# Kernel tuning notes

Measured on AMD Instinct MI355X. Metric: run time of the kernel, lower is better.

Reference implementation:

```python
import jax, jax.numpy as jnp
import numpy as np

B, T, C = 4, 2048, 1024
NH = 16
HS = C // NH


def setup_inputs() -> dict:
    key = jax.random.key(0)
    k1, k2, k3, k4, k5 = jax.random.split(key, 5)
    scale = 1.0 / np.sqrt(C)
    return {
        "x": jax.random.normal(k1, (B, T, C), dtype=jnp.float32),
        "Wk": jax.random.normal(k2, (C, C), dtype=jnp.float32) * scale,
        "Wq": jax.random.normal(k3, (C, C), dtype=jnp.float32) * scale,
        "Wv": jax.random.normal(k4, (C, C), dtype=jnp.float32) * scale,
        "Wp": jax.random.normal(k5, (C, C), dtype=jnp.float32) * scale,
    }


def reference(x, Wk, Wq, Wv, Wp):
    b, t, c = x.shape
    # projections (nn.Linear with bias=False computes x @ W.T; weights here are
    # stored so that x @ W is equivalent -- same math, random init either way)
    k = (x @ Wk).reshape(b, t, NH, HS).transpose(0, 2, 1, 3)  # [B,H,T,hs]
    q = (x @ Wq).reshape(b, t, NH, HS).transpose(0, 2, 1, 3)
    v = (x @ Wv).reshape(b, t, NH, HS).transpose(0, 2, 1, 3)
    att = jnp.einsum("bhqd,bhkd->bhqk", q, k) / jnp.sqrt(jnp.float32(HS))
    causal = jnp.tril(jnp.ones((t, t), dtype=bool))
    att = jnp.where(causal[None, None, :, :], att, -jnp.inf)
    att = jax.nn.softmax(att, axis=-1)
    y = jnp.einsum("bhqk,bhkd->bhqd", att, v)  # [B,H,T,hs]
    y = y.transpose(0, 2, 1, 3).reshape(b, t, c)
    return y @ Wp
```

## Files before the change

kernel.cpp:

```cpp
#include <hip/hip_runtime.h>
#include <cstddef>
#include <cstdint>


namespace {

typedef unsigned short u16;
typedef unsigned int u32;
typedef __attribute__((ext_vector_type(8))) short s8v;
typedef __attribute__((ext_vector_type(4))) short s4v;
typedef __attribute__((ext_vector_type(4))) float f4v;

constexpr int Bn = 4, Tn = 2048, Cn = 1024;
constexpr int Mn = Bn * Tn;
constexpr int KVB = 128;
constexpr int NT128 = Tn / 128;
constexpr float QSCALE = 0.125f * 1.44269504f;

__device__ __forceinline__ u16 bfc(float f) {
  return __builtin_bit_cast(u16, (__bf16)f);
}

__device__ __forceinline__ float ex2(float x) {
#if __has_builtin(__builtin_amdgcn_exp2f)
  return __builtin_amdgcn_exp2f(x);
#else
  return exp2f(x);
#endif
}

__device__ __forceinline__ f4v mfma16(s8v a, s8v b, f4v c) {
  return __builtin_amdgcn_mfma_f32_16x16x32_bf16(a, b, c, 0, 0, 0);
}

__device__ __forceinline__ f4v mfma16k16(s4v a, s4v b, f4v c) {
#if __has_builtin(__builtin_amdgcn_mfma_f32_16x16x16bf16_1k)
  return __builtin_amdgcn_mfma_f32_16x16x16bf16_1k(a, b, c, 0, 0, 0);
#else
  f4v d = c;
  asm("v_mfma_f32_16x16x16_bf16 %0, %1, %2, %0" : "+v"(d) : "v"(a), "v"(b));
  return d;
#endif
}

typedef __attribute__((address_space(1))) const u32 gas_u32;
typedef __attribute__((address_space(3))) u32 las_u32;
__device__ __forceinline__ void gl_lds16(const void* g, void* l) {
  __builtin_amdgcn_global_load_lds((gas_u32*)g, (las_u32*)l, 16, 0, 0);
}

__global__ __launch_bounds__(256) void prep(
    const float* __restrict__ x, u16* __restrict__ xb,
    const float* __restrict__ w0, const float* __restrict__ w1,
    const float* __restrict__ w2, const float* __restrict__ w3,
    u16* __restrict__ o0, u16* __restrict__ o1, u16* __restrict__ o2,
    u16* __restrict__ o3) {
  __shared__ float Tsh[64][65];
  const int bid = blockIdx.x;
  const int tid = threadIdx.x;
  if (bid < 4096) {
    const size_t i = ((size_t)bid * 256 + tid) * 8;
    const float4 a = *(const float4*)(x + i);
    const float4 b = *(const float4*)(x + i + 4);
    alignas(16) u16 t[8] = {bfc(a.x), bfc(a.y), bfc(a.z), bfc(a.w),
                            bfc(b.x), bfc(b.y), bfc(b.z), bfc(b.w)};
    *(s8v*)(xb + i) = *(const s8v*)t;
    return;
  }
  const int idx = bid - 4096;
  const int wz = idx >> 8, wy = (idx >> 4) & 15, wx = idx & 15;
  const float* W;
  u16* O;
  switch (wz) {
    case 0: W = w0; O = o0; break;
    case 1: W = w1; O = o1; break;
    case 2: W = w2; O = o2; break;
    default: W = w3; O = o3; break;
  }
  const int n0 = wx * 64, k0 = wy * 64;
  {
    const int rk = tid >> 2, c0 = (tid & 3) * 16;
#pragma unroll
    for (int u = 0; u < 4; ++u) {
      const float4 v = *(const float4*)&W[(size_t)(k0 + rk) * Cn + n0 + c0 + u * 4];
      Tsh[rk][c0 + u * 4 + 0] = v.x;
      Tsh[rk][c0 + u * 4 + 1] = v.y;
      Tsh[rk][c0 + u * 4 + 2] = v.z;
      Tsh[rk][c0 + u * 4 + 3] = v.w;
    }
  }
  __syncthreads();
  {
    const int rn = tid >> 2, ck0 = (tid & 3) * 16;
    alignas(16) u16 t[16];
#pragma unroll
    for (int u = 0; u < 16; ++u) t[u] = bfc(Tsh[ck0 + u][rn]);
    *(s8v*)&O[(size_t)(n0 + rn) * Cn + k0 + ck0] = *(const s8v*)&t[0];
    *(s8v*)&O[(size_t)(n0 + rn) * Cn + k0 + ck0 + 8] = *(const s8v*)&t[8];
  }
}

template <int OUT_MODE>
__device__ __forceinline__ void gemm_body(const u16* __restrict__ A,
                                          const u16* __restrict__ Bt,
                                          void* __restrict__ Cout, int bm,
                                          int bn, u16* As, u16* Bs) {
  const int N = Cn, K = Cn;
  const int tid = threadIdx.x;
  const int l = tid & 63, w = tid >> 6;
  const int lr = l & 15, lh = l >> 4;
  const int wm = (w >> 1) * 64, wn = (w & 1) * 64;
  const u16* Ab = A + (size_t)(bm * 128) * K;
  const u16* Bb = Bt + (size_t)(bn * 128) * K;
  const int sw = lr & 7;
  f4v acc[4][4] = {};
  for (int k0 = 0; k0 < K; k0 += 64) {
    __syncthreads();
#pragma unroll
    for (int i = 0; i < 4; ++i) {
      const int s = tid + 256 * i;
      const int r = s >> 3, c = s & 7;
      gl_lds16(Ab + (size_t)r * K + k0 + ((c ^ (r & 7)) * 8), &As[s * 8]);
    }
#pragma unroll
    for (int i = 0; i < 4; ++i) {
      const int s = tid + 256 * i;
      const int r = s >> 3, c = s & 7;
      gl_lds16(Bb + (size_t)r * K + k0 + ((c ^ (r & 7)) * 8), &Bs[s * 8]);
    }
    __syncthreads();
#pragma unroll
    for (int half = 0; half < 2; ++half) {
      s8v af[4], bfr[4];
#pragma unroll
      for (int i = 0; i < 4; ++i)
        af[i] = *(const s8v*)&As[(wm + i * 16 + lr) * 64 +
                                 (((half * 4 + lh) ^ sw) * 8)];
#pragma unroll
      for (int j = 0; j < 4; ++j)
        bfr[j] = *(const s8v*)&Bs[(wn + j * 16 + lr) * 64 +
                                  (((half * 4 + lh) ^ sw) * 8)];
      __builtin_amdgcn_s_setprio(1);
#pragma unroll
      for (int i = 0; i < 4; ++i)
#pragma unroll
        for (int j = 0; j < 4; ++j)
          acc[i][j] = mfma16(af[i], bfr[j], acc[i][j]);
      __builtin_amdgcn_s_setprio(0);
    }
  }
  if (OUT_MODE == 2) {
    float* Cf = (float*)Cout;
#pragma unroll
    for (int i = 0; i < 4; ++i) {
      const int row = bm * 128 + wm + i * 16 + lh * 4;
#pragma unroll
      for (int j = 0; j < 4; ++j) {
        const int col = bn * 128 + wn + j * 16 + lr;
#pragma unroll
        for (int r = 0; r < 4; ++r)
          Cf[(size_t)(row + r) * N + col] = acc[i][j][r];
      }
    }
  } else if (OUT_MODE == 0 || OUT_MODE == 3) {
    u16* Cb = (u16*)Cout;
    const float sc = (OUT_MODE == 3) ? QSCALE : 1.0f;
#pragma unroll
    for (int i = 0; i < 4; ++i) {
      const int row = bm * 128 + wm + i * 16 + lh * 4;
#pragma unroll
      for (int j = 0; j < 4; ++j) {
        const int col = bn * 128 + wn + j * 16 + lr;
#pragma unroll
        for (int r = 0; r < 4; ++r)
          Cb[(size_t)(row + r) * N + col] = bfc(acc[i][j][r] * sc);
      }
    }
  } else {
    u16* Vt = (u16*)Cout;
#pragma unroll
    for (int i = 0; i < 4; ++i) {
      const int row0 = bm * 128 + wm + i * 16 + lh * 4;
      const int bq = row0 >> 11;
      const int t0g = row0 & 2047;
      const int tau = t0g & 127;
      const int taup = ((tau >> 5) << 5) | (((tau >> 2) & 3) << 3) |
                       (((tau >> 4) & 1) << 2);
      const int t0p = (t0g & ~127) | taup;
#pragma unroll
      for (int j = 0; j < 4; ++j) {
        const int col = bn * 128 + wn + j * 16 + lr;
        const int hh = col >> 6, dd = col & 63;
        alignas(8) u16 t4[4];
#pragma unroll
        for (int r = 0; r < 4; ++r) t4[r] = bfc(acc[i][j][r]);
        *(s4v*)&Vt[((size_t)((bq * 16 + hh) * 64 + dd)) * Tn + t0p] =
            *(const s4v*)t4;
      }
    }
  }
}

__global__ __launch_bounds__(256) void gemm_qkv(
    const u16* __restrict__ A, const u16* __restrict__ btq,
    const u16* __restrict__ btk, const u16* __restrict__ btv,
    u16* __restrict__ qb, u16* __restrict__ kb, u16* __restrict__ vt) {
  __shared__ __align__(16) u16 As[8192], Bs[8192];
  const int bid = blockIdx.x;
  const int xcd = bid & 7, j = bid >> 3;
  const int bm = xcd * 8 + (j & 7);
  const int combo = j >> 3;
  const int which = combo >> 3, bn = combo & 7;
  if (which == 0)
    gemm_body<3>(A, btq, qb, bm, bn, As, Bs);
  else if (which == 1)
    gemm_body<0>(A, btk, kb, bm, bn, As, Bs);
  else
    gemm_body<1>(A, btv, vt, bm, bn, As, Bs);
}

template <int OUT_MODE>
__global__ __launch_bounds__(256) void gemm_bt(const u16* __restrict__ A,
                                               const u16* __restrict__ Bt,
                                               void* __restrict__ Cout) {
  __shared__ __align__(16) u16 As[8192], Bs[8192];
  const int bid = blockIdx.x;
  const int xcd = bid & 7, j = bid >> 3;
  const int bm = xcd * 8 + (j & 7);
  const int bn = j >> 3;
  gemm_body<OUT_MODE>(A, Bt, Cout, bm, bn, As, Bs);
}

__device__ __forceinline__ void stage_kv(const u16* __restrict__ kgb,
                                         const u16* __restrict__ vtb,
                                         u16* __restrict__ Kb,
                                         u16* __restrict__ Vb, int k0,
                                         int tid) {
#pragma unroll
  for (int is = 0; is < 2; ++is) {
    const int slot = is * 512 + tid;
    const int row = slot >> 3, ch = slot & 7;
    gl_lds16(kgb + (size_t)(k0 + row) * Cn + ((ch ^ (row & 7)) * 8),
             &Kb[slot * 8]);
  }
#pragma unroll
  for (int is = 0; is < 2; ++is) {
    const int slot = is * 512 + tid;
    const int d = slot >> 4, ch = slot & 15;
    gl_lds16(vtb + (size_t)d * Tn + k0 + ((ch ^ (d & 7)) * 8), &Vb[slot * 8]);
  }
}

__device__ __forceinline__ void attn_step(const s8v (&aq)[2],
                                          const u16* __restrict__ Ks,
                                          const u16* __restrict__ Vs, int kb0,
                                          int kb1, const int (&vch)[4], int ln,
                                          int lh, bool diag, int k0, int qg,
                                          float& m_i, float& l_i, f4v* o) {
  f4v s[8] = {};
  __builtin_amdgcn_s_setprio(1);
#pragma unroll
  for (int n = 0; n < 8; ++n) {
    const s8v bk0 = *(const s8v*)&Ks[kb0 + n * 1024];
    const s8v bk1 = *(const s8v*)&Ks[kb1 + n * 1024];
    s[n] = mfma16(bk0, aq[0], s[n]);
    s[n] = mfma16(bk1, aq[1], s[n]);
  }
  __builtin_amdgcn_s_setprio(0);
  float rm = -1e30f;
  if (diag) {
#pragma unroll
    for (int n = 0; n < 8; ++n)
#pragma unroll
      for (int r = 0; r < 4; ++r) {
        float x = s[n][r];
        if (k0 + n * 16 + lh * 4 + r > qg) x = -1e30f;
        s[n][r] = x;
        rm = fmaxf(rm, x);
      }
  } else {
#pragma unroll
    for (int n = 0; n < 8; ++n)
      rm = fmaxf(rm, fmaxf(fmaxf(s[n][0], s[n][1]), fmaxf(s[n][2], s[n][3])));
  }
  if (!__all(rm <= m_i + 11.5f)) {
    float rr = fmaxf(rm, __shfl_xor(rm, 16));
    rr = fmaxf(rr, __shfl_xor(rr, 32));
    const float mnew = fmaxf(m_i, rr);
    const float al = ex2(m_i - mnew);
    m_i = mnew;
    l_i *= al;
#pragma unroll
    for (int r = 0; r < 4; ++r) {
      const float ar = __shfl(al, (ln & 48) | (lh * 4 + r));
#pragma unroll
      for (int n2 = 0; n2 < 4; ++n2) o[n2][r] *= ar;
    }
  }
  s4v pa[8];
  float rs = 0.f;
#pragma unroll
  for (int n = 0; n < 8; ++n) {
    const float p0 = ex2(s[n][0] - m_i);
    const float p1 = ex2(s[n][1] - m_i);
    const float p2 = ex2(s[n][2] - m_i);
    const float p3 = ex2(s[n][3] - m_i);
    rs += (p0 + p1) + (p2 + p3);
    pa[n] = (s4v){(short)bfc(p0), (short)bfc(p1), (short)bfc(p2),
                  (short)bfc(p3)};
  }
  l_i += rs;
  __builtin_amdgcn_s_setprio(1);
#pragma unroll
  for (int n2 = 0; n2 < 4; ++n2) {
#pragma unroll
    for (int p = 0; p < 4; ++p) {
      const s8v vv = *(const s8v*)&Vs[vch[p] + n2 * 2048];
      const s4v lo = {vv[0], vv[1], vv[2], vv[3]};
      const s4v hi = {vv[4], vv[5], vv[6], vv[7]};
      o[n2] = mfma16k16(pa[2 * p], lo, o[n2]);
      o[n2] = mfma16k16(pa[2 * p + 1], hi, o[n2]);
    }
  }
  __builtin_amdgcn_s_setprio(0);
}

__global__ __launch_bounds__(512) void attn_big(const u16* __restrict__ qg,
                                                const u16* __restrict__ kg,
                                                const u16* __restrict__ vtg,
                                                u16* __restrict__ yg) {
  __shared__ __align__(16) u16 Ks0[KVB * 64], Ks1[KVB * 64];
  __shared__ __align__(16) u16 Vs0[64 * KVB], Vs1[64 * KVB];
  const int tid = threadIdx.x;
  const int ln = tid & 63, w = tid >> 6;
  const int lr = ln & 15, lh = ln >> 4;
  const int bid = blockIdx.x;
  const int wg = (bid & 7) * 64 + (bid >> 3);
  const int bh = wg >> 3, xp = wg & 7;
  const int b = bh >> 4, h = bh & 15;
  const int tL = xp, tH = NT128 - 1 - xp;
  const int q0L = tL * 128, q0H = tH * 128;
  const u16* kgb = kg + (size_t)(b * Tn) * Cn + h * 64;
  const u16* vtb = vtg + (size_t)(bh * 64) * Tn;
  const int kb0 = lr * 64 + ((lh) ^ (lr & 7)) * 8;
  const int kb1 = lr * 64 + ((4 + lh) ^ (lr & 7)) * 8;
  int vch[4];
#pragma unroll
  for (int p = 0; p < 4; ++p)
    vch[p] = lr * 128 + ((p * 4 + lh) ^ (lr & 7)) * 8;
  s8v aqL[2], aqH[2];
  {
    const int row = w * 16 + lr;
#pragma unroll
    for (int kd = 0; kd < 2; ++kd) {
      aqL[kd] = *(const s8v*)&qg[(size_t)(b * Tn + q0L + row) * Cn + h * 64 +
                                 kd * 32 + lh * 8];
      aqH[kd] = *(const s8v*)&qg[(size_t)(b * Tn + q0H + row) * Cn + h * 64 +
                                 kd * 32 + lh * 8];
    }
  }
  const int qgH = q0H + w * 16 + lr;
  const int qgL = q0L + w * 16 + lr;
  float mL = -1e30f, lL = 0.f, mH = -1e30f, lH = 0.f;
  f4v oL[4] = {}, oH[4] = {};
  stage_kv(kgb, vtb, Ks0, Vs0, 0, tid);
  __syncthreads();
  for (int kt = 0; kt <= tH; ++kt) {
    const bool cur = kt & 1;
    const u16* Kb = cur ? Ks1 : Ks0;
    const u16* Vb = cur ? Vs1 : Vs0;
    if (kt < tH)
      stage_kv(kgb, vtb, cur ? Ks0 : Ks1, cur ? Vs0 : Vs1, (kt + 1) * KVB,
               tid);
    attn_step(aqH, Kb, Vb, kb0, kb1, vch, ln, lh, kt == tH, kt * KVB, qgH, mH,
              lH, oH);
    if (kt <= tL)
      attn_step(aqL, Kb, Vb, kb0, kb1, vch, ln, lh, kt == tL, kt * KVB, qgL,
                mL, lL, oL);
    __syncthreads();
  }
  {
    float ls = lH;
    ls += __shfl_xor(ls, 16);
    ls += __shfl_xor(ls, 32);
    const float linv = 1.0f / ls;
#pragma unroll
    for (int r = 0; r < 4; ++r) {
      const float iv = __shfl(linv, (ln & 48) | (lh * 4 + r));
      const int row = q0H + w * 16 + lh * 4 + r;
#pragma unroll
      for (int n2 = 0; n2 < 4; ++n2)
        yg[(size_t)(b * Tn + row) * Cn + h * 64 + n2 * 16 + lr] =
            bfc(oH[n2][r] * iv);
    }
  }
  {
    float ls = lL;
    ls += __shfl_xor(ls, 16);
    ls += __shfl_xor(ls, 32);
    const float linv = 1.0f / ls;
#pragma unroll
    for (int r = 0; r < 4; ++r) {
      const float iv = __shfl(linv, (ln & 48) | (lh * 4 + r));
      const int row = q0L + w * 16 + lh * 4 + r;
#pragma unroll
      for (int n2 = 0; n2 < 4; ++n2)
        yg[(size_t)(b * Tn + row) * Cn + h * 64 + n2 * 16 + lr] =
            bfc(oL[n2][r] * iv);
    }
  }
}

}

extern "C" void kernel_launch(void* const* d_in, const int* in_sizes, int n_in,
                              void* d_out, int out_size, void* d_ws,
                              size_t ws_size, hipStream_t stream) {
  (void)in_sizes; (void)n_in; (void)out_size; (void)ws_size;
  const float* x = (const float*)d_in[0];
  const float* Wk = (const float*)d_in[1];
  const float* Wq = (const float*)d_in[2];
  const float* Wv = (const float*)d_in[3];
  const float* Wp = (const float*)d_in[4];
  float* out = (float*)d_out;
  char* ws = (char*)d_ws;

  u16* xb = (u16*)(ws);
  u16* wqt = (u16*)(ws + 16777216);
  u16* wkt = (u16*)(ws + 18874368);
  u16* wvt = (u16*)(ws + 20971520);
  u16* wpt = (u16*)(ws + 23068672);
  u16* qb = (u16*)(ws + 25165824);
  u16* kb = (u16*)(ws + 41943040);
  u16* vt = (u16*)(ws + 58720256);
  u16* yb = (u16*)(ws + 75497472);

  prep<<<dim3(5120), dim3(256), 0, stream>>>(x, xb, Wq, Wk, Wv, Wp, wqt, wkt,
                                             wvt, wpt);
  gemm_qkv<<<dim3(1536), dim3(256), 0, stream>>>(xb, wqt, wkt, wvt, qb, kb,
                                                 vt);
  attn_big<<<dim3(512), dim3(512), 0, stream>>>(qb, kb, vt, yb);
  gemm_bt<2><<<dim3(512), dim3(256), 0, stream>>>(yb, wpt, out);
}
```

Measured before the change: 169.0 us.

## Split paired-tile attention into one query tile per block with 64-key KV tiles

The attention kernel previously had each block handle a low and a high query tile together, sharing 128-key KV tiles between them. Now each block handles one 128-row query tile and streams 64-key K/V tiles, so the grid doubles to 1024 blocks. Blocks are ordered so each XCD group gets a balanced mix of short and long causal tiles. This raises parallelism and halves LDS per block, at the cost of loading K/V once per query tile instead of sharing it across the pair. It also adds more loop iterations and barriers, and the diagonal masking now covers two 64-key tiles.

```diff
diff --git a/kernel.cpp b/kernel.cpp
--- a/kernel.cpp
+++ b/kernel.cpp
@@ -13,8 +13,6 @@
 
 constexpr int Bn = 4, Tn = 2048, Cn = 1024;
 constexpr int Mn = Bn * Tn;
-constexpr int KVB = 128;
-constexpr int NT128 = Tn / 128;
 constexpr float QSCALE = 0.125f * 1.44269504f;
 
 __device__ __forceinline__ u16 bfc(float f) {
@@ -236,31 +234,23 @@
                                          u16* __restrict__ Kb,
                                          u16* __restrict__ Vb, int k0,
                                          int tid) {
-#pragma unroll
-  for (int is = 0; is < 2; ++is) {
-    const int slot = is * 512 + tid;
-    const int row = slot >> 3, ch = slot & 7;
-    gl_lds16(kgb + (size_t)(k0 + row) * Cn + ((ch ^ (row & 7)) * 8),
-             &Kb[slot * 8]);
-  }
-#pragma unroll
-  for (int is = 0; is < 2; ++is) {
-    const int slot = is * 512 + tid;
-    const int d = slot >> 4, ch = slot & 15;
-    gl_lds16(vtb + (size_t)d * Tn + k0 + ((ch ^ (d & 7)) * 8), &Vb[slot * 8]);
-  }
+  const int row = tid >> 3, ch = tid & 7;
+  gl_lds16(kgb + (size_t)(k0 + row) * Cn + ((ch ^ (row & 7)) * 8),
+           &Kb[tid * 8]);
+  gl_lds16(vtb + (size_t)row * Tn + k0 + ((ch ^ (row & 7)) * 8),
+           &Vb[tid * 8]);
 }
 
 __device__ __forceinline__ void attn_step(const s8v (&aq)[2],
                                           const u16* __restrict__ Ks,
                                           const u16* __restrict__ Vs, int kb0,
-                                          int kb1, const int (&vch)[4], int ln,
+                                          int kb1, const int (&vch)[2], int ln,
                                           int lh, bool diag, int k0, int qg,
                                           float& m_i, float& l_i, f4v* o) {
-  f4v s[8] = {};
+  f4v s[4] = {};
   __builtin_amdgcn_s_setprio(1);
 #pragma unroll
-  for (int n = 0; n < 8; ++n) {
+  for (int n = 0; n < 4; ++n) {
     const s8v bk0 = *(const s8v*)&Ks[kb0 + n * 1024];
     const s8v bk1 = *(const s8v*)&Ks[kb1 + n * 1024];
     s[n] = mfma16(bk0, aq[0], s[n]);
@@ -270,7 +260,7 @@
   float rm = -1e30f;
   if (diag) {
 #pragma unroll
-    for (int n = 0; n < 8; ++n)
+    for (int n = 0; n < 4; ++n)
 #pragma unroll
       for (int r = 0; r < 4; ++r) {
         float x = s[n][r];
@@ -280,7 +270,7 @@
       }
   } else {
 #pragma unroll
-    for (int n = 0; n < 8; ++n)
+    for (int n = 0; n < 4; ++n)
       rm = fmaxf(rm, fmaxf(fmaxf(s[n][0], s[n][1]), fmaxf(s[n][2], s[n][3])));
   }
   if (!__all(rm <= m_i + 11.5f)) {
@@ -297,116 +287,98 @@
       for (int n2 = 0; n2 < 4; ++n2) o[n2][r] *= ar;
     }
   }
-  s4v pa[8];
   float rs = 0.f;
-#pragma unroll
-  for (int n = 0; n < 8; ++n) {
-    const float p0 = ex2(s[n][0] - m_i);
-    const float p1 = ex2(s[n][1] - m_i);
-    const float p2 = ex2(s[n][2] - m_i);
-    const float p3 = ex2(s[n][3] - m_i);
-    rs += (p0 + p1) + (p2 + p3);
-    pa[n] = (s4v){(short)bfc(p0), (short)bfc(p1), (short)bfc(p2),
-                  (short)bfc(p3)};
-  }
-  l_i += rs;
   __builtin_amdgcn_s_setprio(1);
 #pragma unroll
-  for (int n2 = 0; n2 < 4; ++n2) {
-#pragma unroll
-    for (int p = 0; p < 4; ++p) {
-      const s8v vv = *(const s8v*)&Vs[vch[p] + n2 * 2048];
+  for (int p = 0; p < 2; ++p) {
+    const float a0 = ex2(s[2 * p][0] - m_i);
+    const float a1 = ex2(s[2 * p][1] - m_i);
+    const float a2 = ex2(s[2 * p][2] - m_i);
+    const float a3 = ex2(s[2 * p][3] - m_i);
+    const float b0 = ex2(s[2 * p + 1][0] - m_i);
+    const float b1 = ex2(s[2 * p + 1][1] - m_i);
+    const float b2 = ex2(s[2 * p + 1][2] - m_i);
+    const float b3 = ex2(s[2 * p + 1][3] - m_i);
+    rs += ((a0 + a1) + (a2 + a3)) + ((b0 + b1) + (b2 + b3));
+    const s4v pa0 = {(short)bfc(a0), (short)bfc(a1), (short)bfc(a2),
+                     (short)bfc(a3)};
+    const s4v pa1 = {(short)bfc(b0), (short)bfc(b1), (short)bfc(b2),
+                     (short)bfc(b3)};
+#pragma unroll
+    for (int n2 = 0; n2 < 4; ++n2) {
+      const s8v vv = *(const s8v*)&Vs[vch[p] + n2 * 1024];
       const s4v lo = {vv[0], vv[1], vv[2], vv[3]};
       const s4v hi = {vv[4], vv[5], vv[6], vv[7]};
-      o[n2] = mfma16k16(pa[2 * p], lo, o[n2]);
-      o[n2] = mfma16k16(pa[2 * p + 1], hi, o[n2]);
+      o[n2] = mfma16k16(pa0, lo, o[n2]);
+      o[n2] = mfma16k16(pa1, hi, o[n2]);
     }
   }
   __builtin_amdgcn_s_setprio(0);
+  l_i += rs;
 }
 
 __global__ __launch_bounds__(512) void attn_big(const u16* __restrict__ qg,
                                                 const u16* __restrict__ kg,
                                                 const u16* __restrict__ vtg,
                                                 u16* __restrict__ yg) {
-  __shared__ __align__(16) u16 Ks0[KVB * 64], Ks1[KVB * 64];
-  __shared__ __align__(16) u16 Vs0[64 * KVB], Vs1[64 * KVB];
+  __shared__ __align__(16) u16 Ks0[4096], Ks1[4096];
+  __shared__ __align__(16) u16 Vs0[4096], Vs1[4096];
   const int tid = threadIdx.x;
   const int ln = tid & 63, w = tid >> 6;
   const int lr = ln & 15, lh = ln >> 4;
   const int bid = blockIdx.x;
-  const int wg = (bid & 7) * 64 + (bid >> 3);
-  const int bh = wg >> 3, xp = wg & 7;
+  const int wg = (bid & 7) * 128 + (bid >> 3);
+  const int xcd = wg >> 7, gl = (wg >> 5) & 3, r5 = wg & 31;
+  const int qt = (gl & 1) ? (15 - (r5 & 7)) : (r5 & 7);
+  const int bh = ((gl >> 1) << 5) | (xcd << 2) | (r5 >> 3);
   const int b = bh >> 4, h = bh & 15;
-  const int tL = xp, tH = NT128 - 1 - xp;
-  const int q0L = tL * 128, q0H = tH * 128;
+  const int q0 = qt * 128;
+  const int nlast = 2 * qt + 1;
   const u16* kgb = kg + (size_t)(b * Tn) * Cn + h * 64;
   const u16* vtb = vtg + (size_t)(bh * 64) * Tn;
   const int kb0 = lr * 64 + ((lh) ^ (lr & 7)) * 8;
   const int kb1 = lr * 64 + ((4 + lh) ^ (lr & 7)) * 8;
-  int vch[4];
-#pragma unroll
-  for (int p = 0; p < 4; ++p)
-    vch[p] = lr * 128 + ((p * 4 + lh) ^ (lr & 7)) * 8;
-  s8v aqL[2], aqH[2];
+  int vch[2];
+#pragma unroll
+  for (int p = 0; p < 2; ++p)
+    vch[p] = lr * 64 + ((p * 4 + lh) ^ (lr & 7)) * 8;
+  s8v aq[2];
   {
-    const int row = w * 16 + lr;
-#pragma unroll
-    for (int kd = 0; kd < 2; ++kd) {
-      aqL[kd] = *(const s8v*)&qg[(size_t)(b * Tn + q0L + row) * Cn + h * 64 +
-                                 kd * 32 + lh * 8];
-      aqH[kd] = *(const s8v*)&qg[(size_t)(b * Tn + q0H + row) * Cn + h * 64 +
-                                 kd * 32 + lh * 8];
-    }
-  }
-  const int qgH = q0H + w * 16 + lr;
-  const int qgL = q0L + w * 16 + lr;
-  float mL = -1e30f, lL = 0.f, mH = -1e30f, lH = 0.f;
-  f4v oL[4] = {}, oH[4] = {};
+    const int row = q0 + w * 16 + lr;
+#pragma unroll
+    for (int kd = 0; kd < 2; ++kd)
+      aq[kd] = *(const s8v*)&qg[(size_t)(b * Tn + row) * Cn + h * 64 +
+                                kd * 32 + lh * 8];
+  }
+  const int qgl = q0 + w * 16 + lr;
+  float m_i = -1e30f, l_i = 0.f;
+  f4v o[4] = {};
   stage_kv(kgb, vtb, Ks0, Vs0, 0, tid);
   __syncthreads();
-  for (int kt = 0; kt <= tH; ++kt) {
+  for (int kt = 0; kt <= nlast; ++kt) {
     const bool cur = kt & 1;
     const u16* Kb = cur ? Ks1 : Ks0;
     const u16* Vb = cur ? Vs1 : Vs0;
-    if (kt < tH)
-      stage_kv(kgb, vtb, cur ? Ks0 : Ks1, cur ? Vs0 : Vs1, (kt + 1) * KVB,
+    if (kt < nlast)
+      stage_kv(kgb, vtb, cur ? Ks0 : Ks1, cur ? Vs0 : Vs1, (kt + 1) * 64,
                tid);
-    attn_step(aqH, Kb, Vb, kb0, kb1, vch, ln, lh, kt == tH, kt * KVB, qgH, mH,
-              lH, oH);
-    if (kt <= tL)
-      attn_step(aqL, Kb, Vb, kb0, kb1, vch, ln, lh, kt == tL, kt * KVB, qgL,
-                mL, lL, oL);
+    attn_step(aq, Kb, Vb, kb0, kb1, vch, ln, lh, kt >= 2 * qt, kt * 64, qgl,
+              m_i, l_i, o);
     __syncthreads();
   }
   {
-    float ls = lH;
+    float ls = l_i;
     ls += __shfl_xor(ls, 16);
     ls += __shfl_xor(ls, 32);
     const float linv = 1.0f / ls;
 #pragma unroll
     for (int r = 0; r < 4; ++r) {
       const float iv = __shfl(linv, (ln & 48) | (lh * 4 + r));
-      const int row = q0H + w * 16 + lh * 4 + r;
+      const int row = q0 + w * 16 + lh * 4 + r;
 #pragma unroll
       for (int n2 = 0; n2 < 4; ++n2)
         yg[(size_t)(b * Tn + row) * Cn + h * 64 + n2 * 16 + lr] =
-            bfc(oH[n2][r] * iv);
-    }
-  }
-  {
-    float ls = lL;
-    ls += __shfl_xor(ls, 16);
-    ls += __shfl_xor(ls, 32);
-    const float linv = 1.0f / ls;
-#pragma unroll
-    for (int r = 0; r < 4; ++r) {
-      const float iv = __shfl(linv, (ln & 48) | (lh * 4 + r));
-      const int row = q0L + w * 16 + lh * 4 + r;
-#pragma unroll
-      for (int n2 = 0; n2 < 4; ++n2)
-        yg[(size_t)(b * Tn + row) * Cn + h * 64 + n2 * 16 + lr] =
-            bfc(oL[n2][r] * iv);
+            bfc(o[n2][r] * iv);
     }
   }
 }
@@ -439,6 +411,6 @@
                                              wvt, wpt);
   gemm_qkv<<<dim3(1536), dim3(256), 0, stream>>>(xb, wqt, wkt, wvt, qb, kb,
                                                  vt);
-  attn_big<<<dim3(512), dim3(512), 0, stream>>>(qb, kb, vt, yb);
+  attn_big<<<dim3(1024), dim3(512), 0, stream>>>(qb, kb, vt, yb);
   gemm_bt<2><<<dim3(512), dim3(256), 0, stream>>>(yb, wpt, out);
 }
```

After: 175.5 us. +3.9%, slower.

## Use 256x128 double-buffered GEMM tiles with interleaved prefetch and MFMA phases

Applied to the files above, without the earlier changes.

Replaces the single-buffered 128x128 GEMM body with a 256x128 tile run by 512 threads (8 waves), double-buffering A and B in LDS. The next k-tile's global-to-LDS loads are issued in chunks between MFMA phases, separated by barriers, so memory transfer overlaps compute instead of stalling on a sync before each tile. Grid sizes and the XCD-aware block mapping are adjusted to match. This raises LDS use to 96KB per block and adds many barriers, which may limit occupancy and leaves fewer blocks for the output projection (256 blocks).

```diff
diff --git a/kernel.cpp b/kernel.cpp
--- a/kernel.cpp
+++ b/kernel.cpp
@@ -12,7 +12,6 @@
 typedef __attribute__((ext_vector_type(4))) float f4v;
 
 constexpr int Bn = 4, Tn = 2048, Cn = 1024;
-constexpr int Mn = Bn * Tn;
 constexpr int KVB = 128;
 constexpr int NT128 = Tn / 128;
 constexpr float QSCALE = 0.125f * 1.44269504f;
@@ -101,59 +100,113 @@
 }
 
 template <int OUT_MODE>
-__device__ __forceinline__ void gemm_body(const u16* __restrict__ A,
-                                          const u16* __restrict__ Bt,
-                                          void* __restrict__ Cout, int bm,
-                                          int bn, u16* As, u16* Bs) {
+__device__ __forceinline__ void gemm_body256(
+    const u16* __restrict__ A, const u16* __restrict__ Bt,
+    void* __restrict__ Cout, int bm, int bn, u16* As0, u16* Bs0, u16* As1,
+    u16* Bs1) {
   const int N = Cn, K = Cn;
   const int tid = threadIdx.x;
   const int l = tid & 63, w = tid >> 6;
   const int lr = l & 15, lh = l >> 4;
   const int wm = (w >> 1) * 64, wn = (w & 1) * 64;
-  const u16* Ab = A + (size_t)(bm * 128) * K;
-  const u16* Bb = Bt + (size_t)(bn * 128) * K;
   const int sw = lr & 7;
+  const u16* Ab = A + (size_t)bm * 256 * K;
+  const u16* Bb = Bt + (size_t)bn * 128 * K;
   f4v acc[4][4] = {};
-  for (int k0 = 0; k0 < K; k0 += 64) {
-    __syncthreads();
-#pragma unroll
-    for (int i = 0; i < 4; ++i) {
-      const int s = tid + 256 * i;
+
+  auto stageA = [&](u16* dst, int k0, int half) {
+#pragma unroll
+    for (int i = 0; i < 2; ++i) {
+      const int s = half * 1024 + i * 512 + tid;
       const int r = s >> 3, c = s & 7;
-      gl_lds16(Ab + (size_t)r * K + k0 + ((c ^ (r & 7)) * 8), &As[s * 8]);
-    }
-#pragma unroll
-    for (int i = 0; i < 4; ++i) {
-      const int s = tid + 256 * i;
+      gl_lds16(Ab + (size_t)r * K + k0 + ((c ^ (r & 7)) * 8), &dst[s * 8]);
+    }
+  };
+  auto stageB = [&](u16* dst, int k0) {
+#pragma unroll
+    for (int i = 0; i < 2; ++i) {
+      const int s = i * 512 + tid;
       const int r = s >> 3, c = s & 7;
-      gl_lds16(Bb + (size_t)r * K + k0 + ((c ^ (r & 7)) * 8), &Bs[s * 8]);
-    }
-    __syncthreads();
-#pragma unroll
-    for (int half = 0; half < 2; ++half) {
-      s8v af[4], bfr[4];
-#pragma unroll
-      for (int i = 0; i < 4; ++i)
-        af[i] = *(const s8v*)&As[(wm + i * 16 + lr) * 64 +
-                                 (((half * 4 + lh) ^ sw) * 8)];
-#pragma unroll
-      for (int j = 0; j < 4; ++j)
-        bfr[j] = *(const s8v*)&Bs[(wn + j * 16 + lr) * 64 +
-                                  (((half * 4 + lh) ^ sw) * 8)];
-      __builtin_amdgcn_s_setprio(1);
-#pragma unroll
-      for (int i = 0; i < 4; ++i)
-#pragma unroll
-        for (int j = 0; j < 4; ++j)
-          acc[i][j] = mfma16(af[i], bfr[j], acc[i][j]);
-      __builtin_amdgcn_s_setprio(0);
-    }
-  }
+      gl_lds16(Bb + (size_t)r * K + k0 + ((c ^ (r & 7)) * 8), &dst[s * 8]);
+    }
+  };
+
+  stageA(As0, 0, 0);
+  stageA(As0, 0, 1);
+  stageB(Bs0, 0);
+  asm volatile("s_waitcnt vmcnt(0)" ::: "memory");
+  __builtin_amdgcn_s_barrier();
+
+  auto ktile = [&](const u16* Ac, const u16* Bc, u16* An, u16* Bnx, int k0n,
+                   bool more) {
+    s8v bfr[4][2];
+#pragma unroll
+    for (int j = 0; j < 4; ++j)
+#pragma unroll
+      for (int kh = 0; kh < 2; ++kh)
+        bfr[j][kh] = *(const s8v*)&Bc[(wn + j * 16 + lr) * 64 +
+                                      (((kh * 4 + lh) ^ sw) * 8)];
+    s8v a0 = *(const s8v*)&Ac[(wm + 0 + lr) * 64 + ((lh ^ sw) * 8)];
+    s8v a1 = *(const s8v*)&Ac[(wm + 16 + lr) * 64 + ((lh ^ sw) * 8)];
+    if (more) stageA(An, k0n, 0);
+    __builtin_amdgcn_s_barrier();
+    __builtin_amdgcn_s_setprio(1);
+#pragma unroll
+    for (int j = 0; j < 4; ++j) {
+      acc[0][j] = mfma16(a0, bfr[j][0], acc[0][j]);
+      acc[1][j] = mfma16(a1, bfr[j][0], acc[1][j]);
+    }
+    __builtin_amdgcn_s_setprio(0);
+    __builtin_amdgcn_s_barrier();
+    a0 = *(const s8v*)&Ac[(wm + 0 + lr) * 64 + (((4 + lh) ^ sw) * 8)];
+    a1 = *(const s8v*)&Ac[(wm + 16 + lr) * 64 + (((4 + lh) ^ sw) * 8)];
+    if (more) stageA(An, k0n, 1);
+    __builtin_amdgcn_s_barrier();
+    __builtin_amdgcn_s_setprio(1);
+#pragma unroll
+    for (int j = 0; j < 4; ++j) {
+      acc[0][j] = mfma16(a0, bfr[j][1], acc[0][j]);
+      acc[1][j] = mfma16(a1, bfr[j][1], acc[1][j]);
+    }
+    __builtin_amdgcn_s_setprio(0);
+    __builtin_amdgcn_s_barrier();
+    a0 = *(const s8v*)&Ac[(wm + 32 + lr) * 64 + ((lh ^ sw) * 8)];
+    a1 = *(const s8v*)&Ac[(wm + 48 + lr) * 64 + ((lh ^ sw) * 8)];
+    if (more) stageB(Bnx, k0n);
+    __builtin_amdgcn_s_barrier();
+    __builtin_amdgcn_s_setprio(1);
+#pragma unroll
+    for (int j = 0; j < 4; ++j) {
+      acc[2][j] = mfma16(a0, bfr[j][0], acc[2][j]);
+      acc[3][j] = mfma16(a1, bfr[j][0], acc[3][j]);
+    }
+    __builtin_amdgcn_s_setprio(0);
+    __builtin_amdgcn_s_barrier();
+    a0 = *(const s8v*)&Ac[(wm + 32 + lr) * 64 + (((4 + lh) ^ sw) * 8)];
+    a1 = *(const s8v*)&Ac[(wm + 48 + lr) * 64 + (((4 + lh) ^ sw) * 8)];
+    asm volatile("s_waitcnt vmcnt(0)" ::: "memory");
+    __builtin_amdgcn_s_barrier();
+    __builtin_amdgcn_s_setprio(1);
+#pragma unroll
+    for (int j = 0; j < 4; ++j) {
+      acc[2][j] = mfma16(a0, bfr[j][1], acc[2][j]);
+      acc[3][j] = mfma16(a1, bfr[j][1], acc[3][j]);
+    }
+    __builtin_amdgcn_s_setprio(0);
+    __builtin_amdgcn_s_barrier();
+  };
+
+  const int NK = K / 64;
+  for (int kt = 0; kt < NK; kt += 2) {
+    ktile(As0, Bs0, As1, Bs1, (kt + 1) * 64, true);
+    ktile(As1, Bs1, As0, Bs0, (kt + 2) * 64, kt + 2 < NK);
+  }
+
   if (OUT_MODE == 2) {
     float* Cf = (float*)Cout;
 #pragma unroll
     for (int i = 0; i < 4; ++i) {
-      const int row = bm * 128 + wm + i * 16 + lh * 4;
+      const int row = bm * 256 + wm + i * 16 + lh * 4;
 #pragma unroll
       for (int j = 0; j < 4; ++j) {
         const int col = bn * 128 + wn + j * 16 + lr;
@@ -167,7 +220,7 @@
     const float sc = (OUT_MODE == 3) ? QSCALE : 1.0f;
 #pragma unroll
     for (int i = 0; i < 4; ++i) {
-      const int row = bm * 128 + wm + i * 16 + lh * 4;
+      const int row = bm * 256 + wm + i * 16 + lh * 4;
 #pragma unroll
       for (int j = 0; j < 4; ++j) {
         const int col = bn * 128 + wn + j * 16 + lr;
@@ -180,7 +233,7 @@
     u16* Vt = (u16*)Cout;
 #pragma unroll
     for (int i = 0; i < 4; ++i) {
-      const int row0 = bm * 128 + wm + i * 16 + lh * 4;
+      const int row0 = bm * 256 + wm + i * 16 + lh * 4;
       const int bq = row0 >> 11;
       const int t0g = row0 & 2047;
       const int tau = t0g & 127;
@@ -201,34 +254,34 @@
   }
 }
 
-__global__ __launch_bounds__(256) void gemm_qkv(
+__global__ __launch_bounds__(512) void gemm_qkv(
     const u16* __restrict__ A, const u16* __restrict__ btq,
     const u16* __restrict__ btk, const u16* __restrict__ btv,
     u16* __restrict__ qb, u16* __restrict__ kb, u16* __restrict__ vt) {
-  __shared__ __align__(16) u16 As[8192], Bs[8192];
+  __shared__ __align__(16) u16 As0[16384], Bs0[8192], As1[16384], Bs1[8192];
   const int bid = blockIdx.x;
-  const int xcd = bid & 7, j = bid >> 3;
-  const int bm = xcd * 8 + (j & 7);
-  const int combo = j >> 3;
+  const int xcd = bid & 7, loc = bid >> 3;
+  const int bm = xcd * 4 + (loc & 3);
+  const int combo = loc >> 2;
   const int which = combo >> 3, bn = combo & 7;
   if (which == 0)
-    gemm_body<3>(A, btq, qb, bm, bn, As, Bs);
+    gemm_body256<3>(A, btq, qb, bm, bn, As0, Bs0, As1, Bs1);
   else if (which == 1)
-    gemm_body<0>(A, btk, kb, bm, bn, As, Bs);
+    gemm_body256<0>(A, btk, kb, bm, bn, As0, Bs0, As1, Bs1);
   else
-    gemm_body<1>(A, btv, vt, bm, bn, As, Bs);
+    gemm_body256<1>(A, btv, vt, bm, bn, As0, Bs0, As1, Bs1);
 }
 
 template <int OUT_MODE>
-__global__ __launch_bounds__(256) void gemm_bt(const u16* __restrict__ A,
+__global__ __launch_bounds__(512) void gemm_bt(const u16* __restrict__ A,
                                                const u16* __restrict__ Bt,
                                                void* __restrict__ Cout) {
-  __shared__ __align__(16) u16 As[8192], Bs[8192];
+  __shared__ __align__(16) u16 As0[16384], Bs0[8192], As1[16384], Bs1[8192];
   const int bid = blockIdx.x;
-  const int xcd = bid & 7, j = bid >> 3;
-  const int bm = xcd * 8 + (j & 7);
-  const int bn = j >> 3;
-  gemm_body<OUT_MODE>(A, Bt, Cout, bm, bn, As, Bs);
+  const int xcd = bid & 7, loc = bid >> 3;
+  const int bm = xcd * 4 + (loc & 3);
+  const int bn = loc >> 2;
+  gemm_body256<OUT_MODE>(A, Bt, Cout, bm, bn, As0, Bs0, As1, Bs1);
 }
 
 __device__ __forceinline__ void stage_kv(const u16* __restrict__ kgb,
@@ -437,8 +490,8 @@
 
   prep<<<dim3(5120), dim3(256), 0, stream>>>(x, xb, Wq, Wk, Wv, Wp, wqt, wkt,
                                              wvt, wpt);
-  gemm_qkv<<<dim3(1536), dim3(256), 0, stream>>>(xb, wqt, wkt, wvt, qb, kb,
-                                                 vt);
+  gemm_qkv<<<dim3(768), dim3(512), 0, stream>>>(xb, wqt, wkt, wvt, qb, kb,
+                                                vt);
   attn_big<<<dim3(512), dim3(512), 0, stream>>>(qb, kb, vt, yb);
-  gemm_bt<2><<<dim3(512), dim3(256), 0, stream>>>(yb, wpt, out);
-}
+  gemm_bt<2><<<dim3(256), dim3(512), 0, stream>>>(yb, wpt, out);
+}
```

Measured after the change: 188.6 us. 1.12x slower.
